# Kernel tuning notes

Measured on AMD Instinct MI355X. Metric: run time of the kernel, lower is better.

## Reference

```python
import jax, jax.numpy as jnp
import numpy as np

N, F_IN, HID, OUT, K, L = 16000, 16, 256, 128, 8, 3


def setup_inputs() -> dict:
    key = jax.random.key(0)
    ks = jax.random.split(key, 8)
    rn = lambda k, sh, sc: (jax.random.normal(k, sh, jnp.float32) * sc)
    return {
        "x": rn(ks[0], (N, F_IN), 1.0),
        "coords": rn(ks[1], (N, 3), 1.0),
        "We": rn(ks[2], (F_IN, HID), 0.1),
        "be": jnp.zeros((HID,), jnp.float32),
        "gnn_W": rn(ks[3], (L, HID, HID), 0.05),
        "gnn_b": jnp.zeros((L, HID), jnp.float32),
        "Wp1": rn(ks[4], (HID, HID // 2), 0.05),
        "bp1": jnp.zeros((HID // 2,), jnp.float32),
        "Wp2": rn(ks[5], (HID // 2, OUT), 0.05),
        "bp2": jnp.zeros((OUT,), jnp.float32),
    }


def knn_edges(coords, k=K):
    # squared pairwise distances (same ordering as torch.cdist) -> kNN, drop self
    sq = jnp.sum(coords * coords, axis=1)
    d2 = sq[:, None] + sq[None, :] - 2.0 * (coords @ coords.T)  # [N, N]
    _, idx = jax.lax.top_k(-d2, k + 1)            # smallest k+1 (incl. self)
    nbr = idx[:, 1:]                               # [N, k]
    src = jnp.broadcast_to(jnp.arange(coords.shape[0])[:, None], nbr.shape)
    return src.reshape(-1), nbr.reshape(-1)       # edge_index rows


def gcn_layer(h, W, b, src, dst, n):
    # GCN with added self-loops and symmetric degree normalization
    deg = jnp.ones((n,), h.dtype).at[dst].add(1.0)   # in-degree + self-loop
    norm = jax.lax.rsqrt(deg)
    hw = h @ W                                        # [N, HID]
    msg = hw[src] * (norm[src] * norm[dst])[:, None]  # gather + scale
    agg = jax.ops.segment_sum(msg, dst, num_segments=n)
    agg = agg + hw * (norm * norm)[:, None]           # self-loop term
    return agg + b


def reference(x, coords, We, be, gnn_W, gnn_b, Wp1, bp1, Wp2, bp2):
    n = x.shape[0]
    src, dst = knn_edges(coords)
    h = x @ We + be                     # survey encoder -> [N, HID]
    for i in range(L):
        h = gcn_layer(h, gnn_W[i], gnn_b[i], src, dst, n)
        h = jax.nn.relu(h)              # dropout is identity in eval mode
    g = jnp.mean(h, axis=0)             # mean pooling (batch=None) -> [HID]
    out = jax.nn.relu(g @ Wp1 + bp1) @ Wp2 + bp2  # output projection -> [OUT]
    return out
```

## Files before the change

kernel.cpp:

```cpp
#include <hip/hip_runtime.h>
#include <math.h>

#define N_NODES 16000
#define F_IN    16
#define HID     256
#define OUTD    128
#define KNN     8
#define LAYERS  3
#define NEDGE   (N_NODES * KNN)

#define NPAD    16384
#define PARTS   4
#define PART_SZ (NPAD / PARTS)
#define SEGS    32
#define NMIN    (PARTS * SEGS)
#define KT      1024
#define CAPP    32

typedef __attribute__((ext_vector_type(8))) short  s8v;
typedef __attribute__((ext_vector_type(4))) float  f4v;

__device__ __forceinline__ unsigned short f2bf(float x) {
    unsigned u = __float_as_uint(x);
    unsigned r = u + 0x7fffu + ((u >> 16) & 1u);
    return (unsigned short)(r >> 16);
}
__device__ __forceinline__ float bf2f(unsigned short b) {
    return __uint_as_float(((unsigned)b) << 16);
}

__global__ __launch_bounds__(256) void prep_kernel(const float* __restrict__ coords,
                                                   float4* __restrict__ cand) {
    int i = blockIdx.x * 256 + threadIdx.x;
    if (i >= NPAD) return;
    if (i < N_NODES) {
        float x = coords[3 * i], y = coords[3 * i + 1], z = coords[3 * i + 2];
        cand[i] = make_float4(-2.f * x, -2.f * y, -2.f * z, x * x + y * y + z * z);
    } else {
        cand[i] = make_float4(0.f, 0.f, 0.f, INFINITY);
    }
}

#define DIST(qx, qy, qz, c) fmaf(qx, c.x, fmaf(qy, c.y, fmaf(qz, c.z, c.w)))

__global__ __launch_bounds__(256) void knn_min_kernel(const float* __restrict__ coords,
                                                      const float4* __restrict__ cand,
                                                      float* __restrict__ minv) {
    __shared__ float4 tile[KT];
    int tid  = threadIdx.x;
    int seg  = tid & 31;
    int qg   = tid >> 5;
    int qbase = blockIdx.x * 64;
    int part = blockIdx.y;

    float qx[8], qy[8], qz[8], m[8];
#pragma unroll
    for (int i = 0; i < 8; ++i) {
        int q = qbase + i * 8 + qg;
        qx[i] = coords[q * 3]; qy[i] = coords[q * 3 + 1]; qz[i] = coords[q * 3 + 2];
        m[i] = INFINITY;
    }

    int pbase = part * PART_SZ;
    for (int t = 0; t < PART_SZ / KT; ++t) {
        __syncthreads();
        for (int l = tid; l < KT; l += 256) tile[l] = cand[pbase + t * KT + l];
        __syncthreads();
#pragma unroll 2
        for (int g = 0; g < KT / 128; ++g) {
            float4 c0 = tile[g * 128 + seg];
            float4 c1 = tile[g * 128 + seg + 32];
            float4 c2 = tile[g * 128 + seg + 64];
            float4 c3 = tile[g * 128 + seg + 96];
#pragma unroll
            for (int i = 0; i < 8; ++i) {
                float d0 = DIST(qx[i], qy[i], qz[i], c0);
                float d1 = DIST(qx[i], qy[i], qz[i], c1);
                float d2 = DIST(qx[i], qy[i], qz[i], c2);
                float d3 = DIST(qx[i], qy[i], qz[i], c3);
                m[i] = fminf(m[i], fminf(fminf(d0, d1), fminf(d2, d3)));
            }
        }
    }
#pragma unroll
    for (int i = 0; i < 8; ++i) {
        int q = qbase + i * 8 + qg;
        minv[(q * PARTS + part) * SEGS + seg] = m[i];
    }
}

__global__ __launch_bounds__(256) void tau_kernel(const float* __restrict__ minv,
                                                  float* __restrict__ tau) {
    int q = blockIdx.x * 256 + threadIdx.x;
    if (q >= N_NODES) return;
    float b[9];
#pragma unroll
    for (int p = 0; p < 9; ++p) b[p] = INFINITY;
    const float4* mv = (const float4*)(minv + (size_t)q * NMIN);
#pragma unroll
    for (int c = 0; c < 16; ++c) {
        float4 a0 = mv[c * 2], a1 = mv[c * 2 + 1];
        float v = fminf(fminf(fminf(a0.x, a0.y), fminf(a0.z, a0.w)),
                        fminf(fminf(a1.x, a1.y), fminf(a1.z, a1.w)));
#pragma unroll
        for (int p = 8; p >= 1; --p) {
            bool  up = v < b[p - 1];
            float nd = up ? b[p - 1] : (v < b[p] ? v : b[p]);
            b[p] = nd;
        }
        if (v < b[0]) b[0] = v;
    }
    tau[q] = b[8];
}

__global__ __launch_bounds__(256) void knn_collect_kernel(const float* __restrict__ coords,
                                                          const float4* __restrict__ cand,
                                                          const float* __restrict__ tau,
                                                          int* __restrict__ cnt,
                                                          float2* __restrict__ cl) {
    __shared__ float4 tile[KT];
    __shared__ int scnt[64];
    int tid  = threadIdx.x;
    int seg  = tid & 31;
    int qg   = tid >> 5;
    int qbase = blockIdx.x * 64;
    int part  = blockIdx.y;

    float qx[8], qy[8], qz[8], tt[8];
#pragma unroll
    for (int i = 0; i < 8; ++i) {
        int q = qbase + i * 8 + qg;
        qx[i] = coords[q * 3]; qy[i] = coords[q * 3 + 1]; qz[i] = coords[q * 3 + 2];
        tt[i] = tau[q];
    }
    if (tid < 64) scnt[tid] = 0;

    int pbase = part * PART_SZ;
    for (int t = 0; t < PART_SZ / KT; ++t) {
        __syncthreads();
        for (int l = tid; l < KT; l += 256) tile[l] = cand[pbase + t * KT + l];
        __syncthreads();
        int gb = pbase + t * KT;
        for (int g = 0; g < KT / 128; ++g) {
            float4 c0 = tile[g * 128 + seg];
            float4 c1 = tile[g * 128 + seg + 32];
            float4 c2 = tile[g * 128 + seg + 64];
            float4 c3 = tile[g * 128 + seg + 96];
            int jb = gb + g * 128 + seg;
#pragma unroll
            for (int i = 0; i < 8; ++i) {
                float d0 = DIST(qx[i], qy[i], qz[i], c0);
                float d1 = DIST(qx[i], qy[i], qz[i], c1);
                float d2 = DIST(qx[i], qy[i], qz[i], c2);
                float d3 = DIST(qx[i], qy[i], qz[i], c3);
                float m4 = fminf(fminf(d0, d1), fminf(d2, d3));
                if (m4 <= tt[i]) {
                    int qi = qbase + i * 8 + qg;
                    int cb = (int)(((size_t)qi * PARTS + part) * CAPP);
                    if (d0 <= tt[i]) {
                        int pos = atomicAdd(&scnt[i * 8 + qg], 1);
                        if (pos < CAPP) cl[cb + pos] = make_float2(d0, __int_as_float(jb));
                    }
                    if (d1 <= tt[i]) {
                        int pos = atomicAdd(&scnt[i * 8 + qg], 1);
                        if (pos < CAPP) cl[cb + pos] = make_float2(d1, __int_as_float(jb + 32));
                    }
                    if (d2 <= tt[i]) {
                        int pos = atomicAdd(&scnt[i * 8 + qg], 1);
                        if (pos < CAPP) cl[cb + pos] = make_float2(d2, __int_as_float(jb + 64));
                    }
                    if (d3 <= tt[i]) {
                        int pos = atomicAdd(&scnt[i * 8 + qg], 1);
                        if (pos < CAPP) cl[cb + pos] = make_float2(d3, __int_as_float(jb + 96));
                    }
                }
            }
        }
    }
    __syncthreads();
    if (tid < 64) cnt[(size_t)(qbase + tid) * PARTS + part] = scnt[tid];
}

#define INS9L(bd, bi, d, j)                                                   \
    {                                                                         \
        _Pragma("unroll")                                                     \
        for (int p = 8; p >= 1; --p) {                                        \
            bool up = (d) < bd[p-1] || ((d) == bd[p-1] && (j) < bi[p-1]);     \
            bool in = (d) < bd[p]   || ((d) == bd[p]   && (j) < bi[p]);       \
            float nd = up ? bd[p-1] : (in ? (d) : bd[p]);                     \
            int   ni = up ? bi[p-1] : (in ? (j) : bi[p]);                     \
            bd[p] = nd; bi[p] = ni;                                           \
        }                                                                     \
        if ((d) < bd[0] || ((d) == bd[0] && (j) < bi[0])) {                   \
            bd[0] = (d); bi[0] = (j);                                         \
        }                                                                     \
    }

__global__ __launch_bounds__(256) void knn_select_kernel(const float* __restrict__ coords,
                                                         const float4* __restrict__ cand,
                                                         const float2* __restrict__ cl,
                                                         const int* __restrict__ cnt,
                                                         int* __restrict__ nbr) {
    int q = blockIdx.x * 256 + threadIdx.x;
    if (q >= N_NODES) return;
    float bd[9]; int bi[9];
#pragma unroll
    for (int p = 0; p < 9; ++p) { bd[p] = INFINITY; bi[p] = 0x7fffffff; }
    int n0 = cnt[(size_t)q * PARTS + 0];
    int n1 = cnt[(size_t)q * PARTS + 1];
    int n2 = cnt[(size_t)q * PARTS + 2];
    int n3 = cnt[(size_t)q * PARTS + 3];
    if (n0 <= CAPP && n1 <= CAPP && n2 <= CAPP && n3 <= CAPP) {
#pragma unroll
        for (int p = 0; p < PARTS; ++p) {
            int n = (p == 0) ? n0 : (p == 1) ? n1 : (p == 2) ? n2 : n3;
            const float2* segp = cl + ((size_t)q * PARTS + p) * CAPP;
            for (int i = 0; i < n; ++i) {
                float2 e = segp[i];
                float d = e.x; int j = __float_as_int(e.y);
                INS9L(bd, bi, d, j);
            }
        }
    } else {
        float qx = coords[q*3], qy = coords[q*3+1], qz = coords[q*3+2];
        for (int j = 0; j < NPAD; ++j) {
            float4 c = cand[j];
            float d = DIST(qx, qy, qz, c);
            if (d < bd[8] || (d == bd[8] && j < bi[8])) INS9L(bd, bi, d, j);
        }
    }
#pragma unroll
    for (int p = 1; p < 9; ++p) nbr[q * 8 + p - 1] = bi[p];
}

__global__ void count_kernel(const int* __restrict__ nbr, int* __restrict__ indeg) {
    int e = blockIdx.x * blockDim.x + threadIdx.x;
    if (e < NEDGE) atomicAdd(&indeg[nbr[e]], 1);
}

__global__ __launch_bounds__(256) void scan_kernel(const int* __restrict__ indeg,
                                                   int* __restrict__ offs,
                                                   float* __restrict__ norm) {
    __shared__ int ssum[256];
    int t = threadIdx.x;
    const int CH = 63;
    int base = t * CH;
    int s = 0;
    for (int c = 0; c < CH; ++c) {
        int idx = base + c;
        if (idx < N_NODES) s += indeg[idx];
    }
    ssum[t] = s;
    __syncthreads();
    for (int d = 1; d < 256; d <<= 1) {
        int v = (t >= d) ? ssum[t - d] : 0;
        __syncthreads();
        ssum[t] += v;
        __syncthreads();
    }
    int run = ssum[t] - s;
    for (int c = 0; c < CH; ++c) {
        int idx = base + c;
        if (idx < N_NODES) {
            int dg = indeg[idx];
            offs[idx] = run;
            run += dg;
            norm[idx] = rsqrtf((float)(1 + dg));
        }
    }
    if (t == 255) offs[N_NODES] = ssum[255];
}

__global__ void fill_kernel(const int* __restrict__ nbr, const int* __restrict__ offs,
                            int* __restrict__ cursor, int* __restrict__ adj) {
    int e = blockIdx.x * blockDim.x + threadIdx.x;
    if (e < NEDGE) {
        int d   = nbr[e];
        int src = e >> 3;
        int pos = atomicAdd(&cursor[d], 1);
        adj[offs[d] + pos] = src;
    }
}

__global__ __launch_bounds__(256) void gemm_kernel(const float* __restrict__ A,
                                                   const float* __restrict__ B,
                                                   float* __restrict__ C,
                                                   int K,
                                                   const float* __restrict__ rowscale,
                                                   const float* __restrict__ bias) {
    __shared__ float As[16][68];
    __shared__ float Bs[16][64];
    int tid = threadIdx.x;
    int rowBase = blockIdx.x * 64;
    int colBase = blockIdx.y * 64;
    int rg = tid >> 4;
    int cg = tid & 15;

    int ar = tid >> 2;
    int ac = (tid & 3) * 4;
    int bk = tid >> 4;
    int bn = (tid & 15) * 4;

    float4 acc0 = {0,0,0,0}, acc1 = {0,0,0,0}, acc2 = {0,0,0,0}, acc3 = {0,0,0,0};

    for (int kb = 0; kb < K; kb += 16) {
        float4 av = *(const float4*)(A + (size_t)(rowBase + ar) * K + kb + ac);
        float4 bv = *(const float4*)(B + (size_t)(kb + bk) * HID + colBase + bn);
        __syncthreads();
        As[ac + 0][ar] = av.x; As[ac + 1][ar] = av.y;
        As[ac + 2][ar] = av.z; As[ac + 3][ar] = av.w;
        *(float4*)&Bs[bk][bn] = bv;
        __syncthreads();
#pragma unroll
        for (int k = 0; k < 16; ++k) {
            float4 a = *(const float4*)&As[k][rg * 4];
            float4 b = *(const float4*)&Bs[k][cg * 4];
            acc0.x = fmaf(a.x, b.x, acc0.x); acc0.y = fmaf(a.x, b.y, acc0.y);
            acc0.z = fmaf(a.x, b.z, acc0.z); acc0.w = fmaf(a.x, b.w, acc0.w);
            acc1.x = fmaf(a.y, b.x, acc1.x); acc1.y = fmaf(a.y, b.y, acc1.y);
            acc1.z = fmaf(a.y, b.z, acc1.z); acc1.w = fmaf(a.y, b.w, acc1.w);
            acc2.x = fmaf(a.z, b.x, acc2.x); acc2.y = fmaf(a.z, b.y, acc2.y);
            acc2.z = fmaf(a.z, b.z, acc2.z); acc2.w = fmaf(a.z, b.w, acc2.w);
            acc3.x = fmaf(a.w, b.x, acc3.x); acc3.y = fmaf(a.w, b.y, acc3.y);
            acc3.z = fmaf(a.w, b.z, acc3.z); acc3.w = fmaf(a.w, b.w, acc3.w);
        }
        __syncthreads();
    }

    int row = rowBase + rg * 4;
    int col = colBase + cg * 4;
    float s0 = 1.f, s1 = 1.f, s2 = 1.f, s3 = 1.f;
    if (rowscale) { s0 = rowscale[row]; s1 = rowscale[row + 1];
                    s2 = rowscale[row + 2]; s3 = rowscale[row + 3]; }
    float4 bb = {0,0,0,0};
    if (bias) bb = *(const float4*)(bias + col);

    float4 v;
    v.x = acc0.x * s0 + bb.x; v.y = acc0.y * s0 + bb.y;
    v.z = acc0.z * s0 + bb.z; v.w = acc0.w * s0 + bb.w;
    *(float4*)(C + (size_t)(row + 0) * HID + col) = v;
    v.x = acc1.x * s1 + bb.x; v.y = acc1.y * s1 + bb.y;
    v.z = acc1.z * s1 + bb.z; v.w = acc1.w * s1 + bb.w;
    *(float4*)(C + (size_t)(row + 1) * HID + col) = v;
    v.x = acc2.x * s2 + bb.x; v.y = acc2.y * s2 + bb.y;
    v.z = acc2.z * s2 + bb.z; v.w = acc2.w * s2 + bb.w;
    *(float4*)(C + (size_t)(row + 2) * HID + col) = v;
    v.x = acc3.x * s3 + bb.x; v.y = acc3.y * s3 + bb.y;
    v.z = acc3.z * s3 + bb.z; v.w = acc3.w * s3 + bb.w;
    *(float4*)(C + (size_t)(row + 3) * HID + col) = v;
}

__global__ __launch_bounds__(256) void wsplit_kernel(const float* __restrict__ W,
                                                     unsigned short* __restrict__ WThi,
                                                     unsigned short* __restrict__ WTlo) {
    int idx = blockIdx.x * 256 + threadIdx.x;
    int l = idx >> 16;
    int r = idx & 65535;
    int k = r >> 8, j = r & 255;
    float x = W[idx];
    unsigned short hb = f2bf(x);
    float hf = bf2f(hb);
    size_t o = (size_t)l * 65536 + j * 256 + k;
    WThi[o] = hb;
    WTlo[o] = f2bf(x - hf);
}

__global__ __launch_bounds__(256) void mfma_gemm_kernel(const float* __restrict__ A,
                                                        const unsigned short* __restrict__ WThi,
                                                        const unsigned short* __restrict__ WTlo,
                                                        unsigned short* __restrict__ C,
                                                        const float* __restrict__ rowscale) {
    __shared__ unsigned short Ahi[64][40], Alo[64][40];
    __shared__ unsigned short Bhi[128][40], Blo[128][40];
    int tid = threadIdx.x;
    int rowBase = blockIdx.x * 64;
    int colBase = blockIdx.y * 128;
    int wave = tid >> 6;
    int lane = tid & 63;
    int fr = lane & 15;
    int fg = lane >> 4;

    int asr = tid >> 2;
    int ask = (tid & 3) * 8;
    int bsj = tid >> 1;
    int bsk = (tid & 1) * 16;

    f4v acc[8];
#pragma unroll
    for (int c = 0; c < 8; ++c) acc[c] = (f4v){0.f, 0.f, 0.f, 0.f};

    for (int kb = 0; kb < HID; kb += 32) {
        const float4* ap = (const float4*)(A + (size_t)(rowBase + asr) * HID + kb + ask);
        float4 a0 = ap[0], a1 = ap[1];
        const uint4* bhp = (const uint4*)(WThi + (size_t)(colBase + bsj) * HID + kb + bsk);
        const uint4* blp = (const uint4*)(WTlo + (size_t)(colBase + bsj) * HID + kb + bsk);
        uint4 bh0 = bhp[0], bh1 = bhp[1];
        uint4 bl0 = blp[0], bl1 = blp[1];

        __syncthreads();
        {
            float xv[8] = {a0.x, a0.y, a0.z, a0.w, a1.x, a1.y, a1.z, a1.w};
            s8v hv, lv;
#pragma unroll
            for (int e = 0; e < 8; ++e) {
                unsigned short hb = f2bf(xv[e]);
                float hf = bf2f(hb);
                hv[e] = (short)hb;
                lv[e] = (short)f2bf(xv[e] - hf);
            }
            *(s8v*)&Ahi[asr][ask] = hv;
            *(s8v*)&Alo[asr][ask] = lv;
        }
        *(uint4*)&Bhi[bsj][bsk]      = bh0;
        *(uint4*)&Bhi[bsj][bsk + 8]  = bh1;
        *(uint4*)&Blo[bsj][bsk]      = bl0;
        *(uint4*)&Blo[bsj][bsk + 8]  = bl1;
        __syncthreads();

        s8v afh = *(s8v*)&Ahi[wave * 16 + fr][fg * 8];
        s8v afl = *(s8v*)&Alo[wave * 16 + fr][fg * 8];
#pragma unroll
        for (int c = 0; c < 8; ++c) {
            s8v bfh = *(s8v*)&Bhi[c * 16 + fr][fg * 8];
            s8v bfl = *(s8v*)&Blo[c * 16 + fr][fg * 8];
            acc[c] = __builtin_amdgcn_mfma_f32_16x16x32_bf16(afh, bfh, acc[c], 0, 0, 0);
            acc[c] = __builtin_amdgcn_mfma_f32_16x16x32_bf16(afh, bfl, acc[c], 0, 0, 0);
            acc[c] = __builtin_amdgcn_mfma_f32_16x16x32_bf16(afl, bfh, acc[c], 0, 0, 0);
        }
    }

    float sc[4];
#pragma unroll
    for (int r = 0; r < 4; ++r) sc[r] = rowscale[rowBase + wave * 16 + fg * 4 + r];
#pragma unroll
    for (int c = 0; c < 8; ++c) {
        int col = colBase + c * 16 + fr;
#pragma unroll
        for (int r = 0; r < 4; ++r) {
            int row = rowBase + wave * 16 + fg * 4 + r;
            C[(size_t)row * HID + col] = f2bf(acc[c][r] * sc[r]);
        }
    }
}

__global__ __launch_bounds__(256) void agg_kernel(const unsigned short* __restrict__ u,
                                                  const float* __restrict__ norm,
                                                  const float* __restrict__ bias,
                                                  const int* __restrict__ offs,
                                                  const int* __restrict__ adj,
                                                  float* __restrict__ hout) {
    int node = blockIdx.x * 4 + (threadIdx.x >> 6);
    int lane = threadIdx.x & 63;
    const ushort4* up = (const ushort4*)u;
    ushort4 sv = up[(size_t)node * 64 + lane];
    float ax = bf2f(sv.x), ay = bf2f(sv.y), az = bf2f(sv.z), aw = bf2f(sv.w);
    int e0 = offs[node], e1 = offs[node + 1];
    for (int e = e0; e < e1; ++e) {
        int s = adj[e];
        ushort4 v = up[(size_t)s * 64 + lane];
        ax += bf2f(v.x); ay += bf2f(v.y); az += bf2f(v.z); aw += bf2f(v.w);
    }
    float nm = norm[node];
    float4 bb = ((const float4*)bias)[lane];
    float4 r;
    r.x = fmaxf(fmaf(nm, ax, bb.x), 0.0f);
    r.y = fmaxf(fmaf(nm, ay, bb.y), 0.0f);
    r.z = fmaxf(fmaf(nm, az, bb.z), 0.0f);
    r.w = fmaxf(fmaf(nm, aw, bb.w), 0.0f);
    ((float4*)hout)[(size_t)node * 64 + lane] = r;
}

__global__ __launch_bounds__(256) void pool_kernel(const float* __restrict__ h,
                                                   float* __restrict__ gsum) {
    int t = threadIdx.x;
    float acc = 0.f;
    int start = blockIdx.x * 250;
    for (int i = 0; i < 250; ++i) acc += h[(size_t)(start + i) * HID + t];
    atomicAdd(&gsum[t], acc);
}

__global__ __launch_bounds__(128) void head_kernel(const float* __restrict__ gsum,
                                                   const float* __restrict__ Wp1,
                                                   const float* __restrict__ bp1,
                                                   const float* __restrict__ Wp2,
                                                   const float* __restrict__ bp2,
                                                   float* __restrict__ out) {
    __shared__ float gl[256];
    __shared__ float hid[128];
    int t = threadIdx.x;
    const float inv = 1.0f / 16000.0f;
    gl[t]       = gsum[t]       * inv;
    gl[t + 128] = gsum[t + 128] * inv;
    __syncthreads();
    float a = bp1[t];
    for (int k = 0; k < 256; ++k) a = fmaf(gl[k], Wp1[k * 128 + t], a);
    hid[t] = fmaxf(a, 0.0f);
    __syncthreads();
    float o = bp2[t];
    for (int k = 0; k < 128; ++k) o = fmaf(hid[k], Wp2[k * 128 + t], o);
    out[t] = o;
}

extern "C" void kernel_launch(void* const* d_in, const int* in_sizes, int n_in,
                              void* d_out, int out_size, void* d_ws, size_t ws_size,
                              hipStream_t stream) {
    const float* x      = (const float*)d_in[0];
    const float* coords = (const float*)d_in[1];
    const float* We     = (const float*)d_in[2];
    const float* be     = (const float*)d_in[3];
    const float* gnn_W  = (const float*)d_in[4];
    const float* gnn_b  = (const float*)d_in[5];
    const float* Wp1    = (const float*)d_in[6];
    const float* bp1    = (const float*)d_in[7];
    const float* Wp2    = (const float*)d_in[8];
    const float* bp2    = (const float*)d_in[9];
    float* out = (float*)d_out;

    char* ws = (char*)d_ws;
    float* h     = (float*)(ws + 0);
    char*  ureg  = ws + 16384000;
    int*   nbr   = (int*)  (ws + 32768000);
    int*   adj   = (int*)  (ws + 33280000);
    int*   indeg = (int*)  (ws + 33792000);
    int*   cursor= (int*)  (ws + 33856000);
    float* gsum  = (float*)(ws + 33920000);
    int*   offs  = (int*)  (ws + 33921024);
    float* norm  = (float*)(ws + 33985152);
    float4* cand = (float4*)(ws + 34049280);

    unsigned short* u16 = (unsigned short*)ureg;
    float*  minv = (float*)ureg;
    float*  tau  = (float*)(ureg + 8192000);
    int*    cnt  = (int*)  (ureg + 8256000);
    unsigned short* WThi = (unsigned short*)(ureg + 8512000);
    unsigned short* WTlo = (unsigned short*)(ureg + 8905216);
    float2* cl   = (float2*)h;

    (void)hipMemsetAsync(ws + 33792000, 0, 129024, stream);

    prep_kernel<<<NPAD / 256, 256, 0, stream>>>(coords, cand);
    knn_min_kernel<<<dim3(N_NODES / 64, PARTS), 256, 0, stream>>>(coords, cand, minv);
    tau_kernel<<<(N_NODES + 255) / 256, 256, 0, stream>>>(minv, tau);
    knn_collect_kernel<<<dim3(N_NODES / 64, PARTS), 256, 0, stream>>>(coords, cand, tau, cnt, cl);
    knn_select_kernel<<<(N_NODES + 255) / 256, 256, 0, stream>>>(coords, cand, cl, cnt, nbr);

    count_kernel<<<(NEDGE + 255) / 256, 256, 0, stream>>>(nbr, indeg);
    scan_kernel<<<1, 256, 0, stream>>>(indeg, offs, norm);
    fill_kernel<<<(NEDGE + 255) / 256, 256, 0, stream>>>(nbr, offs, cursor, adj);

    wsplit_kernel<<<LAYERS * 256, 256, 0, stream>>>(gnn_W, WThi, WTlo);

    dim3 g1(N_NODES / 64, HID / 64);
    gemm_kernel<<<g1, 256, 0, stream>>>(x, We, h, F_IN, nullptr, be);
    for (int l = 0; l < LAYERS; ++l) {
        mfma_gemm_kernel<<<dim3(N_NODES / 64, 2), 256, 0, stream>>>(
            h, WThi + (size_t)l * 65536, WTlo + (size_t)l * 65536, u16, norm);
        agg_kernel<<<N_NODES / 4, 256, 0, stream>>>(u16, norm, gnn_b + (size_t)l * HID,
                                                    offs, adj, h);
    }
    pool_kernel<<<64, 256, 0, stream>>>(h, gsum);
    head_kernel<<<1, 128, 0, stream>>>(gsum, Wp1, bp1, Wp2, bp2, out);
}
```

Measured before the change: 307.1 us.

## Drop LDS tiling in kNN kernels, fuse degree count into select, widen scan

The kNN min and collect kernels now read candidate float4s straight from global memory (via cache) instead of staging 1024-entry tiles in shared memory, which removes the per-tile barriers. The in-degree count moves into the select kernel, so one launch and one pass over nbr go away. The single-block scan grows from 256 to 1024 threads with shorter serial chunks. The cost is that candidate reads now depend on L1/L2 bandwidth rather than LDS, and the scan needs more barrier steps.

```diff
diff --git a/kernel.cpp b/kernel.cpp
--- a/kernel.cpp
+++ b/kernel.cpp
@@ -14,7 +14,6 @@
 #define PART_SZ (NPAD / PARTS)
 #define SEGS    32
 #define NMIN    (PARTS * SEGS)
-#define KT      1024
 #define CAPP    32
 
 typedef __attribute__((ext_vector_type(8))) short  s8v;
@@ -46,7 +45,6 @@
 __global__ __launch_bounds__(256) void knn_min_kernel(const float* __restrict__ coords,
                                                       const float4* __restrict__ cand,
                                                       float* __restrict__ minv) {
-    __shared__ float4 tile[KT];
     int tid  = threadIdx.x;
     int seg  = tid & 31;
     int qg   = tid >> 5;
@@ -62,24 +60,19 @@
     }
 
     int pbase = part * PART_SZ;
-    for (int t = 0; t < PART_SZ / KT; ++t) {
-        __syncthreads();
-        for (int l = tid; l < KT; l += 256) tile[l] = cand[pbase + t * KT + l];
-        __syncthreads();
 #pragma unroll 2
-        for (int g = 0; g < KT / 128; ++g) {
-            float4 c0 = tile[g * 128 + seg];
-            float4 c1 = tile[g * 128 + seg + 32];
-            float4 c2 = tile[g * 128 + seg + 64];
-            float4 c3 = tile[g * 128 + seg + 96];
-#pragma unroll
-            for (int i = 0; i < 8; ++i) {
-                float d0 = DIST(qx[i], qy[i], qz[i], c0);
-                float d1 = DIST(qx[i], qy[i], qz[i], c1);
-                float d2 = DIST(qx[i], qy[i], qz[i], c2);
-                float d3 = DIST(qx[i], qy[i], qz[i], c3);
-                m[i] = fminf(m[i], fminf(fminf(d0, d1), fminf(d2, d3)));
-            }
+    for (int c0 = 0; c0 < PART_SZ; c0 += 128) {
+        float4 v0 = cand[pbase + c0 + seg];
+        float4 v1 = cand[pbase + c0 + seg + 32];
+        float4 v2 = cand[pbase + c0 + seg + 64];
+        float4 v3 = cand[pbase + c0 + seg + 96];
+#pragma unroll
+        for (int i = 0; i < 8; ++i) {
+            float d0 = DIST(qx[i], qy[i], qz[i], v0);
+            float d1 = DIST(qx[i], qy[i], qz[i], v1);
+            float d2 = DIST(qx[i], qy[i], qz[i], v2);
+            float d3 = DIST(qx[i], qy[i], qz[i], v3);
+            m[i] = fminf(m[i], fminf(fminf(d0, d1), fminf(d2, d3)));
         }
     }
 #pragma unroll
@@ -118,7 +111,6 @@
                                                           const float* __restrict__ tau,
                                                           int* __restrict__ cnt,
                                                           float2* __restrict__ cl) {
-    __shared__ float4 tile[KT];
     __shared__ int scnt[64];
     int tid  = threadIdx.x;
     int seg  = tid & 31;
@@ -134,45 +126,40 @@
         tt[i] = tau[q];
     }
     if (tid < 64) scnt[tid] = 0;
+    __syncthreads();
 
     int pbase = part * PART_SZ;
-    for (int t = 0; t < PART_SZ / KT; ++t) {
-        __syncthreads();
-        for (int l = tid; l < KT; l += 256) tile[l] = cand[pbase + t * KT + l];
-        __syncthreads();
-        int gb = pbase + t * KT;
-        for (int g = 0; g < KT / 128; ++g) {
-            float4 c0 = tile[g * 128 + seg];
-            float4 c1 = tile[g * 128 + seg + 32];
-            float4 c2 = tile[g * 128 + seg + 64];
-            float4 c3 = tile[g * 128 + seg + 96];
-            int jb = gb + g * 128 + seg;
-#pragma unroll
-            for (int i = 0; i < 8; ++i) {
-                float d0 = DIST(qx[i], qy[i], qz[i], c0);
-                float d1 = DIST(qx[i], qy[i], qz[i], c1);
-                float d2 = DIST(qx[i], qy[i], qz[i], c2);
-                float d3 = DIST(qx[i], qy[i], qz[i], c3);
-                float m4 = fminf(fminf(d0, d1), fminf(d2, d3));
-                if (m4 <= tt[i]) {
-                    int qi = qbase + i * 8 + qg;
-                    int cb = (int)(((size_t)qi * PARTS + part) * CAPP);
-                    if (d0 <= tt[i]) {
-                        int pos = atomicAdd(&scnt[i * 8 + qg], 1);
-                        if (pos < CAPP) cl[cb + pos] = make_float2(d0, __int_as_float(jb));
-                    }
-                    if (d1 <= tt[i]) {
-                        int pos = atomicAdd(&scnt[i * 8 + qg], 1);
-                        if (pos < CAPP) cl[cb + pos] = make_float2(d1, __int_as_float(jb + 32));
-                    }
-                    if (d2 <= tt[i]) {
-                        int pos = atomicAdd(&scnt[i * 8 + qg], 1);
-                        if (pos < CAPP) cl[cb + pos] = make_float2(d2, __int_as_float(jb + 64));
-                    }
-                    if (d3 <= tt[i]) {
-                        int pos = atomicAdd(&scnt[i * 8 + qg], 1);
-                        if (pos < CAPP) cl[cb + pos] = make_float2(d3, __int_as_float(jb + 96));
-                    }
+    for (int c0 = 0; c0 < PART_SZ; c0 += 128) {
+        float4 v0 = cand[pbase + c0 + seg];
+        float4 v1 = cand[pbase + c0 + seg + 32];
+        float4 v2 = cand[pbase + c0 + seg + 64];
+        float4 v3 = cand[pbase + c0 + seg + 96];
+        int jb = pbase + c0 + seg;
+#pragma unroll
+        for (int i = 0; i < 8; ++i) {
+            float d0 = DIST(qx[i], qy[i], qz[i], v0);
+            float d1 = DIST(qx[i], qy[i], qz[i], v1);
+            float d2 = DIST(qx[i], qy[i], qz[i], v2);
+            float d3 = DIST(qx[i], qy[i], qz[i], v3);
+            float m4 = fminf(fminf(d0, d1), fminf(d2, d3));
+            if (m4 <= tt[i]) {
+                int qi = qbase + i * 8 + qg;
+                int cb = (int)(((size_t)qi * PARTS + part) * CAPP);
+                if (d0 <= tt[i]) {
+                    int pos = atomicAdd(&scnt[i * 8 + qg], 1);
+                    if (pos < CAPP) cl[cb + pos] = make_float2(d0, __int_as_float(jb));
+                }
+                if (d1 <= tt[i]) {
+                    int pos = atomicAdd(&scnt[i * 8 + qg], 1);
+                    if (pos < CAPP) cl[cb + pos] = make_float2(d1, __int_as_float(jb + 32));
+                }
+                if (d2 <= tt[i]) {
+                    int pos = atomicAdd(&scnt[i * 8 + qg], 1);
+                    if (pos < CAPP) cl[cb + pos] = make_float2(d2, __int_as_float(jb + 64));
+                }
+                if (d3 <= tt[i]) {
+                    int pos = atomicAdd(&scnt[i * 8 + qg], 1);
+                    if (pos < CAPP) cl[cb + pos] = make_float2(d3, __int_as_float(jb + 96));
                 }
             }
         }
@@ -200,7 +187,8 @@
                                                          const float4* __restrict__ cand,
                                                          const float2* __restrict__ cl,
                                                          const int* __restrict__ cnt,
-                                                         int* __restrict__ nbr) {
+                                                         int* __restrict__ nbr,
+                                                         int* __restrict__ indeg) {
     int q = blockIdx.x * 256 + threadIdx.x;
     if (q >= N_NODES) return;
     float bd[9]; int bi[9];
@@ -230,20 +218,18 @@
         }
     }
 #pragma unroll
-    for (int p = 1; p < 9; ++p) nbr[q * 8 + p - 1] = bi[p];
-}
-
-__global__ void count_kernel(const int* __restrict__ nbr, int* __restrict__ indeg) {
-    int e = blockIdx.x * blockDim.x + threadIdx.x;
-    if (e < NEDGE) atomicAdd(&indeg[nbr[e]], 1);
-}
-
-__global__ __launch_bounds__(256) void scan_kernel(const int* __restrict__ indeg,
-                                                   int* __restrict__ offs,
-                                                   float* __restrict__ norm) {
-    __shared__ int ssum[256];
+    for (int p = 1; p < 9; ++p) {
+        nbr[q * 8 + p - 1] = bi[p];
+        atomicAdd(&indeg[bi[p]], 1);
+    }
+}
+
+__global__ __launch_bounds__(1024) void scan_kernel(const int* __restrict__ indeg,
+                                                    int* __restrict__ offs,
+                                                    float* __restrict__ norm) {
+    __shared__ int ssum[1024];
     int t = threadIdx.x;
-    const int CH = 63;
+    const int CH = 16;
     int base = t * CH;
     int s = 0;
     for (int c = 0; c < CH; ++c) {
@@ -252,7 +238,7 @@
     }
     ssum[t] = s;
     __syncthreads();
-    for (int d = 1; d < 256; d <<= 1) {
+    for (int d = 1; d < 1024; d <<= 1) {
         int v = (t >= d) ? ssum[t - d] : 0;
         __syncthreads();
         ssum[t] += v;
@@ -268,7 +254,7 @@
             norm[idx] = rsqrtf((float)(1 + dg));
         }
     }
-    if (t == 255) offs[N_NODES] = ssum[255];
+    if (t == 1023) offs[N_NODES] = ssum[1023];
 }
 
 __global__ void fill_kernel(const int* __restrict__ nbr, const int* __restrict__ offs,
@@ -542,10 +528,9 @@
     knn_min_kernel<<<dim3(N_NODES / 64, PARTS), 256, 0, stream>>>(coords, cand, minv);
     tau_kernel<<<(N_NODES + 255) / 256, 256, 0, stream>>>(minv, tau);
     knn_collect_kernel<<<dim3(N_NODES / 64, PARTS), 256, 0, stream>>>(coords, cand, tau, cnt, cl);
-    knn_select_kernel<<<(N_NODES + 255) / 256, 256, 0, stream>>>(coords, cand, cl, cnt, nbr);
-
-    count_kernel<<<(NEDGE + 255) / 256, 256, 0, stream>>>(nbr, indeg);
-    scan_kernel<<<1, 256, 0, stream>>>(indeg, offs, norm);
+    knn_select_kernel<<<(N_NODES + 255) / 256, 256, 0, stream>>>(coords, cand, cl, cnt, nbr, indeg);
+
+    scan_kernel<<<1, 1024, 0, stream>>>(indeg, offs, norm);
     fill_kernel<<<(NEDGE + 255) / 256, 256, 0, stream>>>(nbr, offs, cursor, adj);
 
     wsplit_kernel<<<LAYERS * 256, 256, 0, stream>>>(gnn_W, WThi, WTlo);
```

Result: faster. 294.9 us (-4.0%).
